# Kernel tuning notes

Measured on AMD Instinct MI355X. Metric: run time of the kernel, lower is better.

The kernel has to match this reference:

```python
import jax, jax.numpy as jnp
import numpy as np

NEG_SLOPE = 0.1
N, D = 8192, 256


def setup_inputs() -> dict:
    key = jax.random.key(0)
    ks = jax.random.split(key, 7)
    head = jax.random.normal(ks[0], (N, D), dtype=jnp.float32)
    dependent = jax.random.normal(ks[1], (N, D), dtype=jnp.float32)
    alpha = jax.random.uniform(ks[2], (N, N), dtype=jnp.float32)
    # parameters (torch.rand init -> uniform [0,1))
    agg_weight_head = jax.random.uniform(ks[3], (D, D), dtype=jnp.float32)
    agg_weight_dependent = jax.random.uniform(ks[4], (D, D), dtype=jnp.float32)
    comb_weight_head = jax.random.uniform(ks[5], (D, D), dtype=jnp.float32)
    comb_weight_dependent = jax.random.uniform(ks[6], (D, D), dtype=jnp.float32)
    return {
        "head": head, "dependent": dependent, "alpha": alpha,
        "agg_weight_head": agg_weight_head,
        "agg_weight_dependent": agg_weight_dependent,
        "comb_weight_head": comb_weight_head,
        "comb_weight_dependent": comb_weight_dependent,
    }


def reference(head, dependent, alpha, agg_weight_head, agg_weight_dependent,
              comb_weight_head, comb_weight_dependent):
    # Double loop over j != i is equivalent to dense matmuls with the
    # diagonal contribution subtracted:
    #   head_agg[i]  = sum_j alpha[j,i]*head[j] + alpha[i,j]*dependent[j]  (j != i)
    #   dep_agg[i]   = sum_j alpha[i,j]*head[j] + alpha[j,i]*dependent[j]  (j != i)
    diag = jnp.diagonal(alpha)[:, None]                      # [N,1]
    hd_sum = head + dependent                                # [N,D]
    head_agg = alpha.T @ head + alpha @ dependent - diag * hd_sum
    dep_agg = alpha @ head + alpha.T @ dependent - diag * hd_sum
    head_out = jax.nn.leaky_relu(head_agg @ agg_weight_head + head @ comb_weight_head,
                                 negative_slope=NEG_SLOPE)
    dep_out = jax.nn.leaky_relu(dep_agg @ agg_weight_dependent + dependent @ comb_weight_dependent,
                                negative_slope=NEG_SLOPE)
    return (head_out, dep_out)
```

## Files before the change

### kernel.cpp

```cpp
#include <hip/hip_runtime.h>

#define NN 8192
#define DD 256
#define ND_ (NN * DD)

#define NEG_SLOPE 0.1f

typedef _Float16 half8 __attribute__((ext_vector_type(8)));
typedef _Float16 half4 __attribute__((ext_vector_type(4)));
typedef float f32x4 __attribute__((ext_vector_type(4)));
typedef float f32x16 __attribute__((ext_vector_type(16)));

__device__ __forceinline__ void ld_g2l16(const void* g, void* l) {
    __builtin_amdgcn_global_load_lds(
        (const __attribute__((address_space(1))) void*)g,
        (__attribute__((address_space(3))) void*)l, 16, 0, 0);
}

__device__ __forceinline__ unsigned pkhalf2(_Float16 a, _Float16 b) {
    unsigned short ua = __builtin_bit_cast(unsigned short, a);
    unsigned short ub = __builtin_bit_cast(unsigned short, b);
    return (unsigned)ua | ((unsigned)ub << 16);
}

__global__ __launch_bounds__(256, 2)
void prep_split_kernel(const float* __restrict__ h, const float* __restrict__ d,
                       _Float16* __restrict__ uS_hi, _Float16* __restrict__ vS_hi) {
    __shared__ float s_h[64 * 68];
    __shared__ float s_d[64 * 68];
    const int b  = blockIdx.x;
    const int kt = b >> 2;
    const int ct = b & 3;
    const int k0 = kt * 64;
    const int c0 = ct * 64;
    const int t  = threadIdx.x;

#pragma unroll
    for (int e = 0; e < 4; ++e) {
        int idx = e * 256 + t;
        int r   = idx >> 4;
        int c4  = (idx & 15) << 2;
        float4 hv = *(const float4*)&h[(size_t)(k0 + r) * DD + c0 + c4];
        float4 dv = *(const float4*)&d[(size_t)(k0 + r) * DD + c0 + c4];
        *(float4*)&s_h[r * 68 + c4] = hv;
        *(float4*)&s_d[r * 68 + c4] = dv;
    }
    __syncthreads();

#pragma unroll
    for (int e = 0; e < 2; ++e) {
        int idx = e * 256 + t;
        int c   = idx >> 3;
        int seg = idx & 7;
        half8 uh, vh;
#pragma unroll
        for (int m = 0; m < 8; ++m) {
            float hh = s_h[(seg * 8 + m) * 68 + c];
            float dd = s_d[(seg * 8 + m) * 68 + c];
            uh[m] = (_Float16)(hh + dd);
            vh[m] = (_Float16)(hh - dd);
        }
        int    cg   = c0 + c;
        int    kb   = kt * 2 + (seg >> 2);
        int    slot = (seg & 3) ^ ((cg >> 1) & 3);
        size_t go   = (size_t)kb * 8192 + (size_t)cg * 32 + slot * 8;
        *(half8*)&uS_hi[go] = uh;
        *(half8*)&vS_hi[go] = vh;
    }
}

__global__ __launch_bounds__(512, 2)
void agg_mfma_kernel(const float* __restrict__ alpha,
                     const _Float16* __restrict__ uS_hi, const _Float16* __restrict__ vS_hi,
                     _Float16* __restrict__ Pbuf,
                     _Float16* __restrict__ Qbuf) {
    __shared__ __align__(16) unsigned char smem[106496];

    const int raw  = blockIdx.x;
    const int cb   = (raw >> 3) & 1;
    const int rb   = (raw & 7) | ((raw >> 4) << 3);
    const int I0   = rb * 64;
    const int C0   = cb * 128;
    const int t    = threadIdx.x;
    const int w    = t >> 6;
    const int lane = t & 63;

    const bool isP = (w < 4);
    const int  cw  = w & 3;

    f32x16 acc0, acc1;
#pragma unroll
    for (int r = 0; r < 16; ++r) { acc0[r] = 0.f; acc1[r] = 0.f; }

    const int rbase = t & 15;
    const int kp    = (t >> 4) & 15;
    const int dup   = t >> 8;
    const int row0  = rbase + 32 * dup;
    const int lrow  = lane & 31;
    const int lk    = (lane >> 5) << 3;
    const int c_local = cw * 32 + lrow;

#define LOAD_ALPHA(S, IT)                                                        \
    {                                                                            \
        const int kk0 = (IT) * 64 + 2 * kp;                                      \
        size_t c0off = (size_t)kk0 * NN + I0;                                    \
        S##c00 = alpha[c0off + row0];                                            \
        S##c01 = alpha[c0off + NN + row0];                                       \
        S##c10 = alpha[c0off + row0 + 16];                                       \
        S##c11 = alpha[c0off + NN + row0 + 16];                                  \
        size_t c1off = c0off + (size_t)32 * NN;                                  \
        S##d00 = alpha[c1off + row0];                                            \
        S##d01 = alpha[c1off + NN + row0];                                       \
        S##d10 = alpha[c1off + row0 + 16];                                       \
        S##d11 = alpha[c1off + NN + row0 + 16];                                  \
        S##r00 = *(const float2*)&alpha[(size_t)(I0 + row0) * NN + kk0];         \
        S##r10 = *(const float2*)&alpha[(size_t)(I0 + row0 + 16) * NN + kk0];    \
        S##r01 = *(const float2*)&alpha[(size_t)(I0 + row0) * NN + kk0 + 32];    \
        S##r11 = *(const float2*)&alpha[(size_t)(I0 + row0 + 16) * NN + kk0 + 32]; \
    }

#define ITER(CUR, NXT, P, IT)                                                    \
    {                                                                            \
                                                      \
        LOAD_ALPHA(NXT, (((IT) + 1) & 127))                                      \
        __builtin_amdgcn_sched_barrier(0);                                       \
                   \
        unsigned su0_0 = pkhalf2((_Float16)(CUR##c00 + CUR##r00.x), (_Float16)(CUR##c01 + CUR##r00.y)); \
        unsigned du0_0 = pkhalf2((_Float16)(CUR##c00 - CUR##r00.x), (_Float16)(CUR##c01 - CUR##r00.y)); \
        unsigned su1_0 = pkhalf2((_Float16)(CUR##c10 + CUR##r10.x), (_Float16)(CUR##c11 + CUR##r10.y)); \
        unsigned du1_0 = pkhalf2((_Float16)(CUR##c10 - CUR##r10.x), (_Float16)(CUR##c11 - CUR##r10.y)); \
        unsigned su0_1 = pkhalf2((_Float16)(CUR##d00 + CUR##r01.x), (_Float16)(CUR##d01 + CUR##r01.y)); \
        unsigned du0_1 = pkhalf2((_Float16)(CUR##d00 - CUR##r01.x), (_Float16)(CUR##d01 - CUR##r01.y)); \
        unsigned su1_1 = pkhalf2((_Float16)(CUR##d10 + CUR##r11.x), (_Float16)(CUR##d11 + CUR##r11.y)); \
        unsigned du1_1 = pkhalf2((_Float16)(CUR##d10 - CUR##r11.x), (_Float16)(CUR##d11 - CUR##r11.y)); \
                      \
        {                                                                        \
            unsigned* wS0 = (unsigned*)(smem + (P) * 20480);                     \
            unsigned* wD0 = (unsigned*)(smem + (P) * 20480 + 5120);              \
            unsigned* wS1 = (unsigned*)(smem + (P) * 20480 + 10240);             \
            unsigned* wD1 = (unsigned*)(smem + (P) * 20480 + 15360);             \
            wS0[row0 * 20 + kp]        = su0_0;                                  \
            wS0[(row0 + 16) * 20 + kp] = su1_0;                                  \
            wD0[row0 * 20 + kp]        = du0_0;                                  \
            wD0[(row0 + 16) * 20 + kp] = du1_0;                                  \
            wS1[row0 * 20 + kp]        = su0_1;                                  \
            wS1[(row0 + 16) * 20 + kp] = su1_1;                                  \
            wD1[row0 * 20 + kp]        = du0_1;                                  \
            wD1[(row0 + 16) * 20 + kp] = du1_1;                                  \
        }                                                                        \
        __builtin_amdgcn_sched_barrier(0);                                       \
             \
        asm volatile("s_waitcnt vmcnt(12)" ::: "memory");                        \
        asm volatile("s_waitcnt lgkmcnt(0)" ::: "memory");                       \
        __builtin_amdgcn_s_barrier();                                            \
        __builtin_amdgcn_sched_barrier(0);                                       \
                      \
        {                                                                        \
            size_t gb0 = (size_t)((((IT) + 1) & 127) * 2) * 8192 + cb * 4096 +   \
                         (size_t)(w * 512 + lane * 8);                           \
            unsigned char* bN = smem + 40960 + (1 - (P)) * 32768;                \
            ld_g2l16(uS_hi + gb0,        bN + w * 1024);                         \
            ld_g2l16(vS_hi + gb0,        bN + 8192 + w * 1024);                  \
            ld_g2l16(uS_hi + gb0 + 8192, bN + 16384 + w * 1024);                 \
            ld_g2l16(vS_hi + gb0 + 8192, bN + 24576 + w * 1024);                 \
        }                                                                        \
        __builtin_amdgcn_sched_barrier(0);                                       \
                                    \
        {                                                                        \
            const unsigned char* sdB = smem + (P) * 20480;                       \
            const _Float16* a0p = (const _Float16*)(sdB + (isP ? 0 : 5120));     \
            const _Float16* a1p = (const _Float16*)(sdB + 10240 + (isP ? 0 : 5120)); \
            const unsigned char* bB = smem + 40960 + (P) * 32768;                \
            const _Float16* b0p = (const _Float16*)(bB + (isP ? 0 : 8192));      \
            const _Float16* b1p = (const _Float16*)(bB + 16384 + (isP ? 0 : 8192)); \
            __builtin_amdgcn_s_setprio(1);                                       \
            _Pragma("unroll")                                                    \
            for (int s = 0; s < 2; ++s) {                                        \
                int gd = s * 2 + (lane >> 5);                                    \
                int sl = gd ^ ((c_local >> 1) & 3);                              \
                int bi = c_local * 32 + sl * 8;                                  \
                half8 aH0 = *(const half8*)&a0p[(lrow) * 40 + s * 16 + lk];      \
                half8 aH1 = *(const half8*)&a0p[(32 + lrow) * 40 + s * 16 + lk]; \
                half8 bH  = *(const half8*)&b0p[bi];                             \
                acc0 = __builtin_amdgcn_mfma_f32_32x32x16_f16(aH0, bH, acc0, 0, 0, 0); \
                acc1 = __builtin_amdgcn_mfma_f32_32x32x16_f16(aH1, bH, acc1, 0, 0, 0); \
            }                                                                    \
            _Pragma("unroll")                                                    \
            for (int s = 0; s < 2; ++s) {                                        \
                int gd = s * 2 + (lane >> 5);                                    \
                int sl = gd ^ ((c_local >> 1) & 3);                              \
                int bi = c_local * 32 + sl * 8;                                  \
                half8 aH0 = *(const half8*)&a1p[(lrow) * 40 + s * 16 + lk];      \
                half8 aH1 = *(const half8*)&a1p[(32 + lrow) * 40 + s * 16 + lk]; \
                half8 bH  = *(const half8*)&b1p[bi];                             \
                acc0 = __builtin_amdgcn_mfma_f32_32x32x16_f16(aH0, bH, acc0, 0, 0, 0); \
                acc1 = __builtin_amdgcn_mfma_f32_32x32x16_f16(aH1, bH, acc1, 0, 0, 0); \
            }                                                                    \
            __builtin_amdgcn_s_setprio(0);                                       \
        }                                                                        \
    }

    float Ac00, Ac01, Ac10, Ac11, Ad00, Ad01, Ad10, Ad11;
    float2 Ar00, Ar10, Ar01, Ar11;
    float Bc00, Bc01, Bc10, Bc11, Bd00, Bd01, Bd10, Bd11;
    float2 Br00, Br10, Br01, Br11;

    LOAD_ALPHA(A, 0)
    {
        size_t gb0 = (size_t)(w * 512 + lane * 8) + cb * 4096;
        unsigned char* bN = smem + 40960;
        ld_g2l16(uS_hi + gb0,        bN + w * 1024);
        ld_g2l16(vS_hi + gb0,        bN + 8192 + w * 1024);
        ld_g2l16(uS_hi + gb0 + 8192, bN + 16384 + w * 1024);
        ld_g2l16(vS_hi + gb0 + 8192, bN + 24576 + w * 1024);
    }

    for (int it2 = 0; it2 < 64; ++it2) {
        ITER(A, B, 0, (it2 * 2))
        ITER(B, A, 1, (it2 * 2 + 1))
    }
#undef ITER
#undef LOAD_ALPHA

    _Float16* dst = isP ? Pbuf : Qbuf;
    const int colw = C0 + cw * 32 + (lane & 31);
#pragma unroll
    for (int reg = 0; reg < 16; ++reg) {
        int rr = (reg & 3) + ((reg >> 2) << 3) + ((lane >> 5) << 2);
        dst[(size_t)(I0 + rr) * DD + colw]      = (_Float16)acc0[reg];
        dst[(size_t)(I0 + 32 + rr) * DD + colw] = (_Float16)acc1[reg];
    }
}

__global__ __launch_bounds__(256, 2)
void stageB_kernel(const _Float16* __restrict__ Pbuf, const _Float16* __restrict__ Qbuf,
                   const float* __restrict__ head, const float* __restrict__ dep,
                   const float* __restrict__ alpha,
                   const float* __restrict__ Wah, const float* __restrict__ Wad,
                   const float* __restrict__ Wch, const float* __restrict__ Wcd,
                   float* __restrict__ out) {
    __shared__ float smem2[12544];
    __shared__ float s_dg[64];
    float* s_x  = smem2;
    float* s_y  = smem2 + 2176;
    float* s_w1 = smem2 + 4352;
    float* s_w2 = smem2 + 8448;

    int b   = blockIdx.x;
    int sel = b >> 8;
    int rem = b & 255;
    int rb  = rem >> 1;
    int cb  = rem & 1;
    int I0  = rb * 64;
    int C0  = cb * 128;

    const float* Y  = sel ? dep : head;
    const float* W1 = sel ? Wad : Wah;
    const float* W2 = sel ? Wcd : Wch;
    float* dst = out + sel * ND_;

    int t  = threadIdx.x;
    int rg = t & 15, cg = t >> 4;
    int r0 = rg * 4, c0 = cg * 8;

    if (t < 64) s_dg[t] = alpha[(size_t)(I0 + t) * NN + I0 + t];

    float acc[4][8];
#pragma unroll
    for (int i = 0; i < 4; ++i)
#pragma unroll
        for (int j = 0; j < 8; ++j) acc[i][j] = 0.0f;

    for (int it = 0; it < 8; ++it) {
        int k0 = it * 32;
        __syncthreads();
#pragma unroll
        for (int e = 0; e < 2; ++e) {
            int idx = e * 256 + t;
            int r   = idx >> 3;
            int k4  = (idx & 7) << 2;
            size_t go = (size_t)(I0 + r) * DD + k0 + k4;
            half4 p0 = *(const half4*)&Pbuf[go];
            half4 q0 = *(const half4*)&Qbuf[go];
            float4 hv = *(const float4*)&head[go];
            float4 dv = *(const float4*)&dep[go];
            float dgv = s_dg[r];
            float hj[4] = {hv.x, hv.y, hv.z, hv.w};
            float dj[4] = {dv.x, dv.y, dv.z, dv.w};
#pragma unroll
            for (int j = 0; j < 4; ++j) {
                float Pv = (float)p0[j];
                float Qv = (float)q0[j];
                float uu = hj[j] + dj[j];
                float x  = (sel ? 0.5f * (Pv - Qv) : 0.5f * (Pv + Qv)) - dgv * uu;
                s_x[(k4 + j) * 68 + r] = x;
                s_y[(k4 + j) * 68 + r] = sel ? dj[j] : hj[j];
            }
        }
#pragma unroll
        for (int e = 0; e < 4; ++e) {
            int idx = e * 256 + t;
            int kkk = idx >> 5;
            int c4  = (idx & 31) << 2;
            *(float4*)&s_w1[kkk * 128 + c4] =
                *(const float4*)&W1[(size_t)(k0 + kkk) * DD + C0 + c4];
            *(float4*)&s_w2[kkk * 128 + c4] =
                *(const float4*)&W2[(size_t)(k0 + kkk) * DD + C0 + c4];
        }
        __syncthreads();
#pragma unroll 8
        for (int k = 0; k < 32; ++k) {
            float4 xv = *(const float4*)&s_x[k * 68 + r0];
            float4 yv = *(const float4*)&s_y[k * 68 + r0];
            float4 wa = *(const float4*)&s_w1[k * 128 + c0];
            float4 wb = *(const float4*)&s_w1[k * 128 + c0 + 4];
            float4 wc = *(const float4*)&s_w2[k * 128 + c0];
            float4 wd = *(const float4*)&s_w2[k * 128 + c0 + 4];
            float xs[4]  = {xv.x, xv.y, xv.z, xv.w};
            float ys[4]  = {yv.x, yv.y, yv.z, yv.w};
            float w1s[8] = {wa.x, wa.y, wa.z, wa.w, wb.x, wb.y, wb.z, wb.w};
            float w2s[8] = {wc.x, wc.y, wc.z, wc.w, wd.x, wd.y, wd.z, wd.w};
#pragma unroll
            for (int i = 0; i < 4; ++i)
#pragma unroll
                for (int j = 0; j < 8; ++j)
                    acc[i][j] += xs[i] * w1s[j] + ys[i] * w2s[j];
        }
    }

#pragma unroll
    for (int i = 0; i < 4; ++i) {
#pragma unroll
        for (int jv = 0; jv < 2; ++jv) {
            float4 o;
            float v0 = acc[i][4 * jv + 0];
            float v1 = acc[i][4 * jv + 1];
            float v2 = acc[i][4 * jv + 2];
            float v3 = acc[i][4 * jv + 3];
            o.x = v0 >= 0.0f ? v0 : NEG_SLOPE * v0;
            o.y = v1 >= 0.0f ? v1 : NEG_SLOPE * v1;
            o.z = v2 >= 0.0f ? v2 : NEG_SLOPE * v2;
            o.w = v3 >= 0.0f ? v3 : NEG_SLOPE * v3;
            *(float4*)&dst[(size_t)(I0 + r0 + i) * DD + C0 + c0 + 4 * jv] = o;
        }
    }
}

extern "C" void kernel_launch(void* const* d_in, const int* in_sizes, int n_in,
                              void* d_out, int out_size, void* d_ws, size_t ws_size,
                              hipStream_t stream) {
    const float* head  = (const float*)d_in[0];
    const float* dep   = (const float*)d_in[1];
    const float* alpha = (const float*)d_in[2];
    const float* Wah   = (const float*)d_in[3];
    const float* Wad   = (const float*)d_in[4];
    const float* Wch   = (const float*)d_in[5];
    const float* Wcd   = (const float*)d_in[6];
    float* out = (float*)d_out;

    _Float16* ws    = (_Float16*)d_ws;
    _Float16* uS_hi = ws;
    _Float16* vS_hi = ws + (size_t)ND_;
    _Float16* Pbuf  = ws + (size_t)2 * ND_;
    _Float16* Qbuf  = ws + (size_t)3 * ND_;

    prep_split_kernel<<<512, 256, 0, stream>>>(head, dep, uS_hi, vS_hi);
    agg_mfma_kernel<<<256, 512, 0, stream>>>(alpha, uS_hi, vS_hi, Pbuf, Qbuf);
    stageB_kernel<<<512, 256, 0, stream>>>(Pbuf, Qbuf, head, dep, alpha,
                                           Wah, Wad, Wch, Wcd, out);
}
```

Before: 303.6 us.

## Split aggregation K dimension across two blocks and halve per-iteration tile

Adds a split-K factor of two to the alpha aggregation kernel. Each block now handles half the N reduction range with a 32-wide K step instead of 64, using half the LDS so four blocks can be resident per CU, and the grid doubles to 512 blocks. The two partial P/Q results go to separate fp16 buffers and are summed in stageB. The alpha prefetch now runs two iterations ahead. This trades extra partial-buffer traffic, an extra fp16 rounding of the partials, and more barriers per unit of work for better occupancy and more blocks than CUs.

Result: faster. 282.2 us (-7.0%).

```diff
diff --git a/kernel.cpp b/kernel.cpp
--- a/kernel.cpp
+++ b/kernel.cpp
@@ -69,16 +69,17 @@
     }
 }
 
-__global__ __launch_bounds__(512, 2)
+__global__ __launch_bounds__(512, 4)
 void agg_mfma_kernel(const float* __restrict__ alpha,
                      const _Float16* __restrict__ uS_hi, const _Float16* __restrict__ vS_hi,
                      _Float16* __restrict__ Pbuf,
                      _Float16* __restrict__ Qbuf) {
-    __shared__ __align__(16) unsigned char smem[106496];
+    __shared__ __align__(16) unsigned char smem[53248];
 
     const int raw  = blockIdx.x;
+    const int kh   = raw & 1;
     const int cb   = (raw >> 3) & 1;
-    const int rb   = (raw & 7) | ((raw >> 4) << 3);
+    const int rb   = ((raw >> 1) & 3) | ((raw >> 4) << 2);
     const int I0   = rb * 64;
     const int C0   = cb * 128;
     const int t    = threadIdx.x;
@@ -95,104 +96,72 @@
     const int rbase = t & 15;
     const int kp    = (t >> 4) & 15;
     const int dup   = t >> 8;
-    const int row0  = rbase + 32 * dup;
+    const int rowa  = rbase + 32 * dup;
     const int lrow  = lane & 31;
     const int lk    = (lane >> 5) << 3;
+    const int kbase = kh * (NN / 2);
     const int c_local = cw * 32 + lrow;
 
 #define LOAD_ALPHA(S, IT)                                                        \
     {                                                                            \
-        const int kk0 = (IT) * 64 + 2 * kp;                                      \
-        size_t c0off = (size_t)kk0 * NN + I0;                                    \
-        S##c00 = alpha[c0off + row0];                                            \
-        S##c01 = alpha[c0off + NN + row0];                                       \
-        S##c10 = alpha[c0off + row0 + 16];                                       \
-        S##c11 = alpha[c0off + NN + row0 + 16];                                  \
-        size_t c1off = c0off + (size_t)32 * NN;                                  \
-        S##d00 = alpha[c1off + row0];                                            \
-        S##d01 = alpha[c1off + NN + row0];                                       \
-        S##d10 = alpha[c1off + row0 + 16];                                       \
-        S##d11 = alpha[c1off + NN + row0 + 16];                                  \
-        S##r00 = *(const float2*)&alpha[(size_t)(I0 + row0) * NN + kk0];         \
-        S##r10 = *(const float2*)&alpha[(size_t)(I0 + row0 + 16) * NN + kk0];    \
-        S##r01 = *(const float2*)&alpha[(size_t)(I0 + row0) * NN + kk0 + 32];    \
-        S##r11 = *(const float2*)&alpha[(size_t)(I0 + row0 + 16) * NN + kk0 + 32]; \
-    }
-
-#define ITER(CUR, NXT, P, IT)                                                    \
+        const int kk0 = kbase + (IT) * 32 + 2 * kp;                              \
+        size_t z0 = (size_t)kk0 * NN + I0;                                       \
+        S##c00 = alpha[z0 + rowa];                                               \
+        S##c01 = alpha[z0 + NN + rowa];                                          \
+        S##c10 = alpha[z0 + rowa + 16];                                          \
+        S##c11 = alpha[z0 + NN + rowa + 16];                                     \
+        S##r0  = *(const float2*)&alpha[(size_t)(I0 + rowa) * NN + kk0];         \
+        S##r1  = *(const float2*)&alpha[(size_t)(I0 + rowa + 16) * NN + kk0];    \
+    }
+
+#define ITER(CUR, P, IT)                                                         \
     {                                                                            \
-                                                      \
-        LOAD_ALPHA(NXT, (((IT) + 1) & 127))                                      \
-        __builtin_amdgcn_sched_barrier(0);                                       \
                    \
-        unsigned su0_0 = pkhalf2((_Float16)(CUR##c00 + CUR##r00.x), (_Float16)(CUR##c01 + CUR##r00.y)); \
-        unsigned du0_0 = pkhalf2((_Float16)(CUR##c00 - CUR##r00.x), (_Float16)(CUR##c01 - CUR##r00.y)); \
-        unsigned su1_0 = pkhalf2((_Float16)(CUR##c10 + CUR##r10.x), (_Float16)(CUR##c11 + CUR##r10.y)); \
-        unsigned du1_0 = pkhalf2((_Float16)(CUR##c10 - CUR##r10.x), (_Float16)(CUR##c11 - CUR##r10.y)); \
-        unsigned su0_1 = pkhalf2((_Float16)(CUR##d00 + CUR##r01.x), (_Float16)(CUR##d01 + CUR##r01.y)); \
-        unsigned du0_1 = pkhalf2((_Float16)(CUR##d00 - CUR##r01.x), (_Float16)(CUR##d01 - CUR##r01.y)); \
-        unsigned su1_1 = pkhalf2((_Float16)(CUR##d10 + CUR##r11.x), (_Float16)(CUR##d11 + CUR##r11.y)); \
-        unsigned du1_1 = pkhalf2((_Float16)(CUR##d10 - CUR##r11.x), (_Float16)(CUR##d11 - CUR##r11.y)); \
-                      \
+        unsigned su0 = pkhalf2((_Float16)(CUR##c00 + CUR##r0.x), (_Float16)(CUR##c01 + CUR##r0.y)); \
+        unsigned du0 = pkhalf2((_Float16)(CUR##c00 - CUR##r0.x), (_Float16)(CUR##c01 - CUR##r0.y)); \
+        unsigned su1 = pkhalf2((_Float16)(CUR##c10 + CUR##r1.x), (_Float16)(CUR##c11 + CUR##r1.y)); \
+        unsigned du1 = pkhalf2((_Float16)(CUR##c10 - CUR##r1.x), (_Float16)(CUR##c11 - CUR##r1.y)); \
+                          \
         {                                                                        \
-            unsigned* wS0 = (unsigned*)(smem + (P) * 20480);                     \
-            unsigned* wD0 = (unsigned*)(smem + (P) * 20480 + 5120);              \
-            unsigned* wS1 = (unsigned*)(smem + (P) * 20480 + 10240);             \
-            unsigned* wD1 = (unsigned*)(smem + (P) * 20480 + 15360);             \
-            wS0[row0 * 20 + kp]        = su0_0;                                  \
-            wS0[(row0 + 16) * 20 + kp] = su1_0;                                  \
-            wD0[row0 * 20 + kp]        = du0_0;                                  \
-            wD0[(row0 + 16) * 20 + kp] = du1_0;                                  \
-            wS1[row0 * 20 + kp]        = su0_1;                                  \
-            wS1[(row0 + 16) * 20 + kp] = su1_1;                                  \
-            wD1[row0 * 20 + kp]        = du0_1;                                  \
-            wD1[(row0 + 16) * 20 + kp] = du1_1;                                  \
+            unsigned* wS = (unsigned*)(smem + (P) * 10240);                      \
+            unsigned* wD = (unsigned*)(smem + (P) * 10240 + 5120);               \
+            wS[rowa * 20 + kp]        = su0;                                     \
+            wS[(rowa + 16) * 20 + kp] = su1;                                     \
+            wD[rowa * 20 + kp]        = du0;                                     \
+            wD[(rowa + 16) * 20 + kp] = du1;                                     \
         }                                                                        \
-        __builtin_amdgcn_sched_barrier(0);                                       \
-             \
-        asm volatile("s_waitcnt vmcnt(12)" ::: "memory");                        \
+               \
+        asm volatile("s_waitcnt vmcnt(6)" ::: "memory");                         \
         asm volatile("s_waitcnt lgkmcnt(0)" ::: "memory");                       \
         __builtin_amdgcn_s_barrier();                                            \
         __builtin_amdgcn_sched_barrier(0);                                       \
-                      \
+           \
         {                                                                        \
-            size_t gb0 = (size_t)((((IT) + 1) & 127) * 2) * 8192 + cb * 4096 +   \
-                         (size_t)(w * 512 + lane * 8);                           \
-            unsigned char* bN = smem + 40960 + (1 - (P)) * 32768;                \
-            ld_g2l16(uS_hi + gb0,        bN + w * 1024);                         \
-            ld_g2l16(vS_hi + gb0,        bN + 8192 + w * 1024);                  \
-            ld_g2l16(uS_hi + gb0 + 8192, bN + 16384 + w * 1024);                 \
-            ld_g2l16(vS_hi + gb0 + 8192, bN + 24576 + w * 1024);                 \
+            size_t gb = (size_t)(kh * 128 + (((IT) + 1) & 127)) * 8192 +         \
+                        cb * 4096 + (size_t)(w * 512 + lane * 8);                \
+            unsigned char* bN = smem + 20480 + (1 - (P)) * 16384;                \
+            ld_g2l16(uS_hi + gb, bN + w * 1024);                                 \
+            ld_g2l16(vS_hi + gb, bN + 8192 + w * 1024);                          \
         }                                                                        \
+        __builtin_amdgcn_sched_barrier(0);         \
+                 \
+        LOAD_ALPHA(CUR, (((IT) + 2) & 127))                                      \
         __builtin_amdgcn_sched_barrier(0);                                       \
                                     \
         {                                                                        \
-            const unsigned char* sdB = smem + (P) * 20480;                       \
-            const _Float16* a0p = (const _Float16*)(sdB + (isP ? 0 : 5120));     \
-            const _Float16* a1p = (const _Float16*)(sdB + 10240 + (isP ? 0 : 5120)); \
-            const unsigned char* bB = smem + 40960 + (P) * 32768;                \
-            const _Float16* b0p = (const _Float16*)(bB + (isP ? 0 : 8192));      \
-            const _Float16* b1p = (const _Float16*)(bB + 16384 + (isP ? 0 : 8192)); \
+            const unsigned char* sd = smem + (P) * 10240;                        \
+            const _Float16* aSD = (const _Float16*)(sd + (isP ? 0 : 5120));      \
+            const unsigned char* bb = smem + 20480 + (P) * 16384;                \
+            const _Float16* bB  = (const _Float16*)(bb + (isP ? 0 : 8192));      \
             __builtin_amdgcn_s_setprio(1);                                       \
             _Pragma("unroll")                                                    \
             for (int s = 0; s < 2; ++s) {                                        \
                 int gd = s * 2 + (lane >> 5);                                    \
                 int sl = gd ^ ((c_local >> 1) & 3);                              \
                 int bi = c_local * 32 + sl * 8;                                  \
-                half8 aH0 = *(const half8*)&a0p[(lrow) * 40 + s * 16 + lk];      \
-                half8 aH1 = *(const half8*)&a0p[(32 + lrow) * 40 + s * 16 + lk]; \
-                half8 bH  = *(const half8*)&b0p[bi];                             \
-                acc0 = __builtin_amdgcn_mfma_f32_32x32x16_f16(aH0, bH, acc0, 0, 0, 0); \
-                acc1 = __builtin_amdgcn_mfma_f32_32x32x16_f16(aH1, bH, acc1, 0, 0, 0); \
-            }                                                                    \
-            _Pragma("unroll")                                                    \
-            for (int s = 0; s < 2; ++s) {                                        \
-                int gd = s * 2 + (lane >> 5);                                    \
-                int sl = gd ^ ((c_local >> 1) & 3);                              \
-                int bi = c_local * 32 + sl * 8;                                  \
-                half8 aH0 = *(const half8*)&a1p[(lrow) * 40 + s * 16 + lk];      \
-                half8 aH1 = *(const half8*)&a1p[(32 + lrow) * 40 + s * 16 + lk]; \
-                half8 bH  = *(const half8*)&b1p[bi];                             \
+                half8 aH0 = *(const half8*)&aSD[(lrow) * 40 + s * 16 + lk];      \
+                half8 aH1 = *(const half8*)&aSD[(32 + lrow) * 40 + s * 16 + lk]; \
+                half8 bH  = *(const half8*)&bB[bi];                              \
                 acc0 = __builtin_amdgcn_mfma_f32_32x32x16_f16(aH0, bH, acc0, 0, 0, 0); \
                 acc1 = __builtin_amdgcn_mfma_f32_32x32x16_f16(aH1, bH, acc1, 0, 0, 0); \
             }                                                                    \
@@ -200,29 +169,29 @@
         }                                                                        \
     }
 
-    float Ac00, Ac01, Ac10, Ac11, Ad00, Ad01, Ad10, Ad11;
-    float2 Ar00, Ar10, Ar01, Ar11;
-    float Bc00, Bc01, Bc10, Bc11, Bd00, Bd01, Bd10, Bd11;
-    float2 Br00, Br10, Br01, Br11;
+    float Ac00, Ac01, Ac10, Ac11;
+    float2 Ar0, Ar1;
+    float Bc00, Bc01, Bc10, Bc11;
+    float2 Br0, Br1;
 
     LOAD_ALPHA(A, 0)
+    LOAD_ALPHA(B, 1)
     {
-        size_t gb0 = (size_t)(w * 512 + lane * 8) + cb * 4096;
-        unsigned char* bN = smem + 40960;
-        ld_g2l16(uS_hi + gb0,        bN + w * 1024);
-        ld_g2l16(vS_hi + gb0,        bN + 8192 + w * 1024);
-        ld_g2l16(uS_hi + gb0 + 8192, bN + 16384 + w * 1024);
-        ld_g2l16(vS_hi + gb0 + 8192, bN + 24576 + w * 1024);
+        size_t gb = (size_t)(kh * 128) * 8192 + cb * 4096 +
+                    (size_t)(w * 512 + lane * 8);
+        unsigned char* bN = smem + 20480;
+        ld_g2l16(uS_hi + gb, bN + w * 1024);
+        ld_g2l16(vS_hi + gb, bN + 8192 + w * 1024);
     }
 
     for (int it2 = 0; it2 < 64; ++it2) {
-        ITER(A, B, 0, (it2 * 2))
-        ITER(B, A, 1, (it2 * 2 + 1))
+        ITER(A, 0, (it2 * 2))
+        ITER(B, 1, (it2 * 2 + 1))
     }
 #undef ITER
 #undef LOAD_ALPHA
 
-    _Float16* dst = isP ? Pbuf : Qbuf;
+    _Float16* dst = (isP ? Pbuf : Qbuf) + (size_t)kh * ND_;
     const int colw = C0 + cw * 32 + (lane & 31);
 #pragma unroll
     for (int reg = 0; reg < 16; ++reg) {
@@ -281,7 +250,9 @@
             int k4  = (idx & 7) << 2;
             size_t go = (size_t)(I0 + r) * DD + k0 + k4;
             half4 p0 = *(const half4*)&Pbuf[go];
+            half4 p1 = *(const half4*)&Pbuf[ND_ + go];
             half4 q0 = *(const half4*)&Qbuf[go];
+            half4 q1 = *(const half4*)&Qbuf[ND_ + go];
             float4 hv = *(const float4*)&head[go];
             float4 dv = *(const float4*)&dep[go];
             float dgv = s_dg[r];
@@ -289,8 +260,8 @@
             float dj[4] = {dv.x, dv.y, dv.z, dv.w};
 #pragma unroll
             for (int j = 0; j < 4; ++j) {
-                float Pv = (float)p0[j];
-                float Qv = (float)q0[j];
+                float Pv = (float)p0[j] + (float)p1[j];
+                float Qv = (float)q0[j] + (float)q1[j];
                 float uu = hj[j] + dj[j];
                 float x  = (sel ? 0.5f * (Pv - Qv) : 0.5f * (Pv + Qv)) - dgv * uu;
                 s_x[(k4 + j) * 68 + r] = x;
@@ -362,10 +333,10 @@
     _Float16* uS_hi = ws;
     _Float16* vS_hi = ws + (size_t)ND_;
     _Float16* Pbuf  = ws + (size_t)2 * ND_;
-    _Float16* Qbuf  = ws + (size_t)3 * ND_;
+    _Float16* Qbuf  = ws + (size_t)4 * ND_;
 
     prep_split_kernel<<<512, 256, 0, stream>>>(head, dep, uS_hi, vS_hi);
-    agg_mfma_kernel<<<256, 512, 0, stream>>>(alpha, uS_hi, vS_hi, Pbuf, Qbuf);
+    agg_mfma_kernel<<<512, 512, 0, stream>>>(alpha, uS_hi, vS_hi, Pbuf, Qbuf);
     stageB_kernel<<<512, 256, 0, stream>>>(Pbuf, Qbuf, head, dep, alpha,
                                            Wah, Wad, Wch, Wcd, out);
 }
```
